# Kernel optimization log

Hardware: AMD Instinct MI355X
Metric: run time of the kernel (lower is better)

The kernel has to match this reference:

```python
import jax, jax.numpy as jnp
import numpy as np

KNN = 16
EPS = 1e-5

def _bn(x, g, b):
    # BatchNorm2d over channel-last axis, training-mode batch stats (axes B,N,K)
    m = jnp.mean(x, axis=(0, 1, 2), keepdims=True)
    v = jnp.var(x, axis=(0, 1, 2), keepdims=True)
    return (x - m) * jax.lax.rsqrt(v + EPS) * g + b

def _gather(x, idx):
    # x [B,N,C], idx [B,...] -> [B,...,C]
    return jax.vmap(lambda xi, ii: xi[ii])(x, idx)

def _fps(pc, m):
    # deterministic farthest point sampling starting at index 0 -> [B,m] int32
    B, N, _ = pc.shape
    first = jnp.zeros((B,), jnp.int32)
    def body(carry, _):
        mind, last = carry
        lp = jnp.take_along_axis(pc, last[:, None, None], axis=1)  # [B,1,3]
        mind = jnp.minimum(mind, jnp.sum((pc - lp) ** 2, axis=-1))  # [B,N]
        nxt = jnp.argmax(mind, axis=-1).astype(jnp.int32)
        return (mind, nxt), nxt
    _, rest = jax.lax.scan(body, (jnp.full((B, N), 1e10, pc.dtype), first), None, length=m - 1)
    return jnp.concatenate([first[None], rest], axis=0).T  # [B,m]

def _knn(pc1, pc2, k):
    # squared-distance matrix + k smallest (sorted ascending) -> indices [B,N1,k]
    d = (jnp.sum(pc1 ** 2, -1)[:, :, None] + jnp.sum(pc2 ** 2, -1)[:, None, :]
         - 2.0 * jnp.einsum('bnc,bmc->bnm', pc1, pc2))
    return jax.lax.top_k(-d, k)[1]

def reference(dec_x, dec_pc, enc_x, enc_pc,
              W_pre1, b_pre1, W_pre2, b_pre2,
              Wq, bq, Wk, bk, Wv, bv,
              Wp1, bp1, gp, betap, Wp2, bp2,
              Wa1, ba1, ga, betaa, Wa2, ba2,
              W_post1, b_post1, W_post2, b_post2):
    residue = dec_x
    dx = dec_x @ W_pre1 + b_pre1
    ex = enc_x @ W_pre2 + b_pre2
    pc = jnp.concatenate([dec_pc, enc_pc], axis=1)
    xx = jnp.concatenate([dx, ex], axis=1)
    fidx = _fps(pc, dec_pc.shape[1])
    pc = _gather(pc, fidx)
    xx = _gather(xx, fidx)
    q = dx @ Wq + bq
    k = xx @ Wk + bk
    v = xx @ Wv + bv
    nidx = _knn(dec_pc, pc, KNN)                          # [B,N1,K]
    pos_in = _gather(pc, nidx) - dec_pc[:, :, None, :]    # [B,N1,K,3] relative pos
    k = _gather(k, nidx)                                  # [B,N1,K,D]
    v = _gather(v, nidx)
    pos = jax.nn.relu(_bn(pos_in @ Wp1 + bp1, gp, betap)) @ Wp2 + bp2
    attn = k - q[:, :, None, :] + pos
    attn = jax.nn.relu(_bn(attn @ Wa1 + ba1, ga, betaa)) @ Wa2 + ba2
    attn = jax.nn.softmax(attn, axis=-2)                  # softmax over K neighbors
    x = jnp.sum((v + pos) * attn, axis=2)                 # [B,N1,D]
    return (x @ W_post1 + b_post1 + residue, dec_pc, x @ W_post2 + b_post2, enc_pc)

def setup_inputs():
    B, N1, N2 = 4, 2048, 2048
    D, I1, I2, HP, HA = 256, 256, 256, 64, 64
    ks = jax.random.split(jax.random.key(0), 24)
    rn = lambda i, shp, s: jax.random.normal(ks[i], shp, jnp.float32) * s
    z = lambda n: jnp.zeros((n,), jnp.float32)
    o = lambda n: jnp.ones((n,), jnp.float32)
    return {
        'dec_x': rn(0, (B, N1, I1), 1.0),
        'dec_pc': jax.random.uniform(ks[1], (B, N1, 3), jnp.float32),
        'enc_x': rn(2, (B, N2, I2), 1.0),
        'enc_pc': jax.random.uniform(ks[3], (B, N2, 3), jnp.float32),
        'W_pre1': rn(4, (I1, D), 0.02), 'b_pre1': z(D),
        'W_pre2': rn(5, (I2, D), 0.02), 'b_pre2': z(D),
        'Wq': rn(6, (D, D), 0.02), 'bq': z(D),
        'Wk': rn(7, (D, D), 0.02), 'bk': z(D),
        'Wv': rn(8, (D, D), 0.02), 'bv': z(D),
        'Wp1': rn(9, (3, HP), 0.1), 'bp1': z(HP), 'gp': o(HP), 'betap': z(HP),
        'Wp2': rn(10, (HP, D), 0.02), 'bp2': z(D),
        'Wa1': rn(11, (D, HA), 0.02), 'ba1': z(HA), 'ga': o(HA), 'betaa': z(HA),
        'Wa2': rn(12, (HA, D), 0.02), 'ba2': z(D),
        'W_post1': rn(13, (D, I1), 0.02), 'b_post1': z(I1),
        'W_post2': rn(14, (D, I2), 0.02), 'b_post2': z(I2),
    }
```

## Files before the change

kernel.cpp:

```cpp
#include <hip/hip_runtime.h>
#include <hip/hip_bf16.h>


typedef __hip_bfloat16 bf16;

__device__ __forceinline__ float b2f(bf16 x){ return __bfloat162float(x); }
__device__ __forceinline__ bf16  f2b(float x){ return __float2bfloat16(x); }

#define NQ    8192
#define NSAMP 131072

__global__ void detect_dtype(const unsigned int* __restrict__ words,
                             int* __restrict__ flag)
{
  int i = blockIdx.x*256 + threadIdx.x;
  unsigned int w = words[i];
  float v = __uint_as_float((w & 0xffffu) << 16);
  if (!(fabsf(v) <= 1e3f)) atomicOr(flag, 1);
}

struct ConvArgs {
  const void* src[30];
  float*      dst[30];
  int         n[30];
};
__global__ void convert_inputs(ConvArgs a, const int* __restrict__ flag)
{
  int t = blockIdx.y;
  int n = a.n[t];
  int isf32 = *flag;
  const void* s = a.src[t];
  float* d = a.dst[t];
  for (int i = blockIdx.x*256 + threadIdx.x; i < n; i += gridDim.x*256) {
    d[i] = isf32 ? ((const float*)s)[i] : b2f(((const bf16*)s)[i]);
  }
}

__global__ void copy_f32(const float* __restrict__ src, float* __restrict__ dst, int n)
{
  int i = blockIdx.x*256 + threadIdx.x;
  if (i < n) dst[i] = src[i];
}

template<int CTRL>
__device__ __forceinline__ void dpp_step(float& d, int& i) {
  int sd = __builtin_amdgcn_update_dpp(__float_as_int(d), __float_as_int(d),
                                       CTRL, 0xf, 0xf, false);
  int si = __builtin_amdgcn_update_dpp(i, i, CTRL, 0xf, 0xf, false);
  float fd = __int_as_float(sd);
  bool take = (fd > d) || (fd == d && si < i);
  d = take ? fd : d;
  i = take ? si : i;
}

__global__ __launch_bounds__(256) void fps_kernel(
    const float* __restrict__ dec_pc, const float* __restrict__ enc_pc,
    int* __restrict__ fidx)
{
  int b = blockIdx.x;
  int tid = threadIdx.x;
  __shared__ float4 spc[4096];
  __shared__ float  cd[2][4];
  __shared__ int    ci[2][4];

  float px[16], py[16], pz[16], mind[16];
#pragma unroll
  for (int i = 0; i < 16; ++i) {
    int p = tid*16 + i;
    const float* s = (p < 2048) ? dec_pc + ((size_t)b*2048 + p)*3
                                : enc_pc + ((size_t)b*2048 + (p-2048))*3;
    px[i] = s[0]; py[i] = s[1]; pz[i] = s[2];
    spc[p] = make_float4(px[i], py[i], pz[i], 0.f);
    mind[i] = 1e10f;
  }
  if (tid == 0) fidx[(size_t)b*2048] = 0;
  __syncthreads();

  int last = 0;
  int wv = tid >> 6;
  for (int t = 1; t < 2048; ++t) {
    float4 lp = spc[last];
    float bv = -1.f; int bi = 0x7fffffff;
#pragma unroll
    for (int i = 0; i < 16; ++i) {
      float ddx = px[i]-lp.x, ddy = py[i]-lp.y, ddz = pz[i]-lp.z;
      float d = __fadd_rn(__fadd_rn(__fmul_rn(ddx,ddx), __fmul_rn(ddy,ddy)),
                          __fmul_rn(ddz,ddz));
      mind[i] = fminf(mind[i], d);
      if (mind[i] > bv) { bv = mind[i]; bi = tid*16 + i; }
    }
    dpp_step<0x111>(bv, bi);
    dpp_step<0x112>(bv, bi);
    dpp_step<0x114>(bv, bi);
    dpp_step<0x118>(bv, bi);
    dpp_step<0x142>(bv, bi);
    dpp_step<0x143>(bv, bi);
    float wd = __int_as_float(__builtin_amdgcn_readlane(__float_as_int(bv), 63));
    int   wi = __builtin_amdgcn_readlane(bi, 63);
    int par = t & 1;
    if ((tid & 63) == 0) { cd[par][wv] = wd; ci[par][wv] = wi; }
    __syncthreads();
    float bd2 = cd[par][0]; int bi2 = ci[par][0];
#pragma unroll
    for (int w = 1; w < 4; ++w) {
      float d2 = cd[par][w]; int i2 = ci[par][w];
      if (d2 > bd2 || (d2 == bd2 && i2 < bi2)) { bd2 = d2; bi2 = i2; }
    }
    last = bi2;
    if (tid == 0) fidx[(size_t)b*2048 + t] = bi2;
  }
}

__global__ void gather_pc_kernel(const float* __restrict__ dec_pc,
                                 const float* __restrict__ enc_pc,
                                 const int* __restrict__ fidx,
                                 float* __restrict__ pcs)
{
  int i = blockIdx.x*256 + threadIdx.x;
  if (i >= NQ) return;
  int b = i >> 11;
  int g = fidx[i];
  const float* s = (g < 2048) ? dec_pc + ((size_t)b*2048 + g)*3
                              : enc_pc + ((size_t)b*2048 + (g-2048))*3;
  float X = s[0], Y = s[1], Z = s[2];
  float s2 = __fadd_rn(__fadd_rn(__fmul_rn(X,X), __fmul_rn(Y,Y)), __fmul_rn(Z,Z));
  ((float4*)pcs)[i] = make_float4(X, Y, Z, s2);
}

__global__ __launch_bounds__(64) void knn_kernel(
    const float* __restrict__ dec_pc, const float* __restrict__ pcs,
    int* __restrict__ nidx)
{
  int gq = blockIdx.x*64 + threadIdx.x;
  if (gq >= NQ) return;
  int b = gq >> 11;
  float qx = dec_pc[(size_t)gq*3+0];
  float qy = dec_pc[(size_t)gq*3+1];
  float qz = dec_pc[(size_t)gq*3+2];
  float s1 = __fadd_rn(__fadd_rn(__fmul_rn(qx,qx), __fmul_rn(qy,qy)), __fmul_rn(qz,qz));
  float bd[16]; int bi[16];
#pragma unroll
  for (int i = 0; i < 16; ++i) { bd[i] = 3.4e38f; bi[i] = 0; }
  const float4* P = (const float4*)(pcs) + (size_t)b*2048;
  for (int j = 0; j < 2048; ++j) {
    float4 p = P[j];
    float inner = __fadd_rn(__fadd_rn(__fmul_rn(qx,p.x), __fmul_rn(qy,p.y)),
                            __fmul_rn(qz,p.z));
    float d = __fsub_rn(__fadd_rn(s1, p.w), __fmul_rn(2.f, inner));
    if (d < bd[15]) {
      bd[15] = d; bi[15] = j;
#pragma unroll
      for (int k = 15; k >= 1; --k) {
        if (bd[k] < bd[k-1]) {
          float td = bd[k]; bd[k] = bd[k-1]; bd[k-1] = td;
          int   ti = bi[k]; bi[k] = bi[k-1]; bi[k-1] = ti;
        }
      }
    }
  }
  int* o = nidx + (size_t)gq*16;
#pragma unroll
  for (int i = 0; i < 16; ++i) o[i] = bi[i];
}

template<bool RESID>
__global__ __launch_bounds__(256) void gemm256(
    const float* __restrict__ A, const float* __restrict__ W,
    const float* __restrict__ bias, const float* __restrict__ resid,
    float* __restrict__ C, int M, int N)
{
  __shared__ float As[16][68];
  __shared__ float Bs[16][68];
  int bm = blockIdx.x*64, bn = blockIdx.y*64;
  int tid = threadIdx.x;
  int tr = tid >> 4, tc = tid & 15;
  float acc[4][4] = {};
  for (int k0 = 0; k0 < 256; k0 += 16) {
#pragma unroll
    for (int i = 0; i < 4; ++i) {
      int idx = tid + i*256;
      int m = idx >> 4, k = idx & 15;
      As[k][m] = A[(size_t)(bm+m)*256 + k0 + k];
    }
#pragma unroll
    for (int i = 0; i < 4; ++i) {
      int idx = tid + i*256;
      int k = idx >> 6, n = idx & 63;
      Bs[k][n] = W[(size_t)(k0+k)*N + bn + n];
    }
    __syncthreads();
#pragma unroll
    for (int k = 0; k < 16; ++k) {
      float4 a4 = *(const float4*)&As[k][tr*4];
      float4 b4 = *(const float4*)&Bs[k][tc*4];
      float a[4] = {a4.x, a4.y, a4.z, a4.w};
      float b[4] = {b4.x, b4.y, b4.z, b4.w};
#pragma unroll
      for (int i = 0; i < 4; ++i)
#pragma unroll
        for (int j = 0; j < 4; ++j) acc[i][j] += a[i]*b[j];
    }
    __syncthreads();
  }
#pragma unroll
  for (int i = 0; i < 4; ++i) {
    int m = bm + tr*4 + i;
#pragma unroll
    for (int j = 0; j < 4; ++j) {
      int n = bn + tc*4 + j;
      float v = acc[i][j] + (bias ? bias[n] : 0.f);
      if (RESID) v += resid[(size_t)m*N + n];
      C[(size_t)m*N + n] = v;
    }
  }
}

__global__ void gather_rows(const float* __restrict__ dx,
                            const float* __restrict__ ex,
                            const int* __restrict__ fidx,
                            float* __restrict__ xxg)
{
  int r = blockIdx.x;
  int b = r >> 11;
  int g = fidx[r];
  const float* src = (g < 2048) ? dx + ((size_t)(b*2048 + g))*256
                                : ex + ((size_t)(b*2048 + g - 2048))*256;
  ((float4*)(xxg + (size_t)r*256))[threadIdx.x] = ((const float4*)src)[threadIdx.x];
}

__global__ void fold_wa1(const float* __restrict__ Wq, const float* __restrict__ bq,
                         const float* __restrict__ Wk, const float* __restrict__ bk,
                         const float* __restrict__ Wa1,
                         float* __restrict__ Wqa, float* __restrict__ Wka,
                         float* __restrict__ bqa, float* __restrict__ bka)
{
  int c = threadIdx.x;
  int r = blockIdx.x;
  float aq = 0.f, ak = 0.f;
  if (r < 256) {
    for (int j = 0; j < 256; ++j) {
      float w = Wa1[j*64+c];
      aq += Wq[r*256+j]*w; ak += Wk[r*256+j]*w;
    }
    Wqa[r*64+c] = aq; Wka[r*64+c] = ak;
  } else {
    for (int j = 0; j < 256; ++j) {
      float w = Wa1[j*64+c];
      aq += bq[j]*w; ak += bk[j]*w;
    }
    bqa[c] = aq; bka[c] = ak;
  }
}

__global__ __launch_bounds__(256) void bn1_stats(
    const float* __restrict__ dec_pc, const float* __restrict__ pcs,
    const int* __restrict__ nidx, const float* __restrict__ Wp1,
    const float* __restrict__ bp1, double* __restrict__ sums)
{
  __shared__ float pin[256][3];
  __shared__ float red[8][64];
  int tid = threadIdx.x;
  int s0 = blockIdx.x * 256;
  {
    int s = s0 + tid;
    int qrow = s >> 4;
    int b = s >> 15;
    int g = nidx[s];
    float4 p = ((const float4*)pcs)[(size_t)b*2048 + g];
    pin[tid][0] = p.x - dec_pc[(size_t)qrow*3+0];
    pin[tid][1] = p.y - dec_pc[(size_t)qrow*3+1];
    pin[tid][2] = p.z - dec_pc[(size_t)qrow*3+2];
  }
  __syncthreads();
  int c = tid & 63, grp = tid >> 6;
  float w0 = Wp1[c], w1 = Wp1[64+c], w2 = Wp1[128+c], bb = bp1[c];
  float sm = 0.f, sq = 0.f;
  for (int i = 0; i < 64; ++i) {
    int r = grp*64 + i;
    float h = pin[r][0]*w0 + pin[r][1]*w1 + pin[r][2]*w2 + bb;
    sm += h; sq += h*h;
  }
  red[grp][c] = sm; red[4+grp][c] = sq;
  __syncthreads();
  if (tid < 64) {
    atomicAdd(&sums[tid], (double)(red[0][tid]+red[1][tid]+red[2][tid]+red[3][tid]));
  } else if (tid < 128) {
    int c2 = tid - 64;
    atomicAdd(&sums[64+c2], (double)(red[4][c2]+red[5][c2]+red[6][c2]+red[7][c2]));
  }
}

__global__ void bn_fin(const double* __restrict__ sums,
                       const float* __restrict__ gamma, const float* __restrict__ beta,
                       float* __restrict__ ab)
{
  int c = threadIdx.x;
  double mean = sums[c]    * (1.0/131072.0);
  double var  = sums[64+c] * (1.0/131072.0) - mean*mean;
  double inv  = 1.0 / sqrt(var + 1e-5);
  float a  = (float)(gamma[c] * inv);
  float bb = (float)(beta[c] - mean * (double)a);
  ab[c] = a; ab[64+c] = bb;
}

__global__ __launch_bounds__(256) void ph_kernel(
    const float* __restrict__ dec_pc, const float* __restrict__ pcs,
    const int* __restrict__ nidx, const float* __restrict__ Wp1,
    const float* __restrict__ bp1, const float* __restrict__ ab,
    bf16* __restrict__ PH)
{
  __shared__ float pin[256][3];
  int tid = threadIdx.x;
  int s0 = blockIdx.x * 256;
  {
    int s = s0 + tid;
    int qrow = s >> 4;
    int b = s >> 15;
    int g = nidx[s];
    float4 p = ((const float4*)pcs)[(size_t)b*2048 + g];
    pin[tid][0] = p.x - dec_pc[(size_t)qrow*3+0];
    pin[tid][1] = p.y - dec_pc[(size_t)qrow*3+1];
    pin[tid][2] = p.z - dec_pc[(size_t)qrow*3+2];
  }
  __syncthreads();
  int c = tid & 63, grp = tid >> 6;
  float w0 = Wp1[c], w1 = Wp1[64+c], w2 = Wp1[128+c], bb = bp1[c];
  float a = ab[c], sh = ab[64+c];
  for (int i = 0; i < 64; ++i) {
    int r = grp*64 + i;
    int s = s0 + r;
    float h = pin[r][0]*w0 + pin[r][1]*w1 + pin[r][2]*w2 + bb;
    PH[(size_t)s*64 + c] = f2b(fmaxf(h*a + sh, 0.f));
  }
}

__global__ void wprime_c1(const float* __restrict__ Wp2, const float* __restrict__ Wa1,
                          const float* __restrict__ bp2, const float* __restrict__ ba1,
                          float* __restrict__ Wpr, float* __restrict__ c1)
{
  int c = threadIdx.x;
  int r = blockIdx.x;
  if (r < 64) {
    float acc = 0.f;
    for (int e = 0; e < 256; ++e) acc += Wp2[r*256+e] * Wa1[e*64+c];
    Wpr[r*64+c] = acc;
  } else {
    float acc = ba1[c];
    for (int e = 0; e < 256; ++e) acc += bp2[e] * Wa1[e*64+c];
    c1[c] = acc;
  }
}

__global__ __launch_bounds__(256) void bn2_stats(
    const bf16* __restrict__ PH, const float* __restrict__ Wpr,
    const float* __restrict__ ka, const float* __restrict__ qa,
    const float* __restrict__ c1v, const int* __restrict__ nidx,
    bf16* __restrict__ attnpre, double* __restrict__ sums)
{
  __shared__ float phT[64][68];
  __shared__ float wp[64][68];
  __shared__ float red[16][64];
  __shared__ float red2[16][64];
  int tid = threadIdx.x;
  int s0 = blockIdx.x * 64;
#pragma unroll
  for (int i = 0; i < 16; ++i) {
    int idx = tid + i*256;
    wp[idx>>6][idx&63] = Wpr[idx];
    int r = idx >> 6, d = idx & 63;
    phT[d][r] = b2f(PH[(size_t)(s0+r)*64 + d]);
  }
  __syncthreads();
  int tr = tid >> 4, tc = tid & 15;
  float acc[4][4] = {};
#pragma unroll 8
  for (int d = 0; d < 64; ++d) {
    float4 a4 = *(const float4*)&phT[d][tr*4];
    float4 b4 = *(const float4*)&wp[d][tc*4];
    float a[4] = {a4.x, a4.y, a4.z, a4.w};
    float b[4] = {b4.x, b4.y, b4.z, b4.w};
#pragma unroll
    for (int i = 0; i < 4; ++i)
#pragma unroll
      for (int j = 0; j < 4; ++j) acc[i][j] += a[i]*b[j];
  }
  float psum[4] = {0,0,0,0}, psq[4] = {0,0,0,0};
#pragma unroll
  for (int i = 0; i < 4; ++i) {
    int r = tr*4 + i;
    int s = s0 + r;
    int b = s >> 15;
    int g = nidx[s];
    int qrow = s >> 4;
    const float* karow = ka + ((size_t)b*2048 + g)*64;
    const float* qarow = qa + (size_t)qrow*64;
#pragma unroll
    for (int j = 0; j < 4; ++j) {
      int c = tc*4 + j;
      float v = acc[i][j] + karow[c] - qarow[c] + c1v[c];
      attnpre[(size_t)s*64 + c] = f2b(v);
      psum[j] += v; psq[j] += v*v;
    }
  }
#pragma unroll
  for (int j = 0; j < 4; ++j) { red[tr][tc*4+j] = psum[j]; red2[tr][tc*4+j] = psq[j]; }
  __syncthreads();
  if (tid < 64) {
    float t = 0.f, t2 = 0.f;
#pragma unroll
    for (int i = 0; i < 16; ++i) { t += red[i][tid]; t2 += red2[i][tid]; }
    atomicAdd(&sums[tid], (double)t);
    atomicAdd(&sums[64+tid], (double)t2);
  }
}

__global__ __launch_bounds__(256) void final_attn(
    const bf16* __restrict__ attnpre, const bf16* __restrict__ PH,
    const float* __restrict__ ab2,
    const float* __restrict__ Wa2, const float* __restrict__ ba2,
    const float* __restrict__ Wp2, const float* __restrict__ bp2,
    const float* __restrict__ vsb, const int* __restrict__ nidx,
    float* __restrict__ xout)
{
  int tid = threadIdx.x;
  float wa[64], wpc[64];
#pragma unroll
  for (int d = 0; d < 64; ++d) {
    wa[d]  = Wa2[d*256 + tid];
    wpc[d] = Wp2[d*256 + tid];
  }
  float cba2 = ba2[tid];
  float cbp2 = bp2[tid];
  __shared__ float th[16][64];
  __shared__ float ph[16][64];
  __shared__ int   sn[16];
  for (int qi = 0; qi < 16; ++qi) {
    int q = blockIdx.x*16 + qi;
#pragma unroll
    for (int i = 0; i < 4; ++i) {
      int idx = tid + i*256;
      int k = idx >> 6, d = idx & 63;
      size_t gi = (size_t)q*1024 + idx;
      th[k][d] = fmaxf(b2f(attnpre[gi])*ab2[d] + ab2[64+d], 0.f);
      ph[k][d] = b2f(PH[gi]);
    }
    if (tid < 16) sn[tid] = nidx[(size_t)q*16 + tid];
    __syncthreads();
    float av[16], pv[16];
#pragma unroll
    for (int k = 0; k < 16; ++k) {
      float sa = cba2, sp = cbp2;
#pragma unroll
      for (int d = 0; d < 64; d += 4) {
        float4 t4 = *(const float4*)&th[k][d];
        float4 p4 = *(const float4*)&ph[k][d];
        sa += t4.x*wa[d] + t4.y*wa[d+1] + t4.z*wa[d+2] + t4.w*wa[d+3];
        sp += p4.x*wpc[d] + p4.y*wpc[d+1] + p4.z*wpc[d+2] + p4.w*wpc[d+3];
      }
      av[k] = sa; pv[k] = sp;
    }
    float m = av[0];
#pragma unroll
    for (int k = 1; k < 16; ++k) m = fmaxf(m, av[k]);
    float den = 0.f, num = 0.f;
    int b = q >> 11;
#pragma unroll
    for (int k = 0; k < 16; ++k) {
      float e = __expf(av[k] - m);
      den += e;
      float vk = vsb[((size_t)(b*2048 + sn[k]))*256 + tid];
      num += (vk + pv[k]) * e;
    }
    xout[(size_t)q*256 + tid] = num / den;
    __syncthreads();
  }
}

extern "C" void kernel_launch(void* const* d_in, const int* in_sizes, int n_in,
                              void* d_out, int out_size, void* d_ws, size_t ws_size,
                              hipStream_t stream) {
  (void)in_sizes; (void)n_in; (void)out_size; (void)ws_size;
  char* ws = (char*)d_ws;

  float* dec_xF  = (float*)(ws + 0);
  float* enc_xF  = (float*)(ws + 8388608);
  float* dxb     = (float*)(ws + 16777216);
  float* exb     = (float*)(ws + 25165824);
  float* Wqa     = (float*)(ws + 33554432);
  float* Wka     = (float*)(ws + 33619968);
  float* bqa     = (float*)(ws + 33685504);
  float* bka     = (float*)(ws + 33685760);
  float* xxg     = (float*)(ws + 41943040);
  float* vsb     = (float*)(ws + 58720256);
  float* xb      = (float*)(ws + 67108864);
  bf16*  PHb     = (bf16*)(ws + 75497472);
  bf16*  apre    = (bf16*)(ws + 92274688);
  float* qab     = (float*)(ws + 109051904);
  float* kab     = (float*)(ws + 111149056);
  float* dec_pcF = (float*)(ws + 113246208);
  float* enc_pcF = (float*)(ws + 113344512);
  float* W_pre1F = (float*)(ws + 113442816);
  float* W_pre2F = (float*)(ws + 113704960);
  float* WqF     = (float*)(ws + 113967104);
  float* WkF     = (float*)(ws + 114229248);
  float* WvF     = (float*)(ws + 114491392);
  float* W_post1F= (float*)(ws + 114753536);
  float* W_post2F= (float*)(ws + 115015680);
  float* Wp2F    = (float*)(ws + 115277824);
  float* Wa1F    = (float*)(ws + 115343360);
  float* Wa2F    = (float*)(ws + 115408896);
  float* Wp1F    = (float*)(ws + 115474432);
  float* vecs    = (float*)(ws + 115475456);
  float* b_pre1F = vecs + 0*256;
  float* b_pre2F = vecs + 1*256;
  float* bqF     = vecs + 2*256;
  float* bkF     = vecs + 3*256;
  float* bvF     = vecs + 4*256;
  float* bp1F    = vecs + 5*256;
  float* gpF     = vecs + 6*256;
  float* betapF  = vecs + 7*256;
  float* bp2F    = vecs + 8*256;
  float* ba1F    = vecs + 9*256;
  float* gaF     = vecs + 10*256;
  float* betaaF  = vecs + 11*256;
  float* ba2F    = vecs + 12*256;
  float* b_post1F= vecs + 13*256;
  float* b_post2F= vecs + 14*256;
  float* pcs     = (float*)(ws + 115490816);
  int*   fidx    = (int*)(ws + 115621888);
  int*   nidx    = (int*)(ws + 115654656);
  double* sums   = (double*)(ws + 116178944);
  float* Wpr     = (float*)(ws + 116180992);
  float* c1v     = (float*)(ws + 116197376);
  float* a1b1    = (float*)(ws + 116197632);
  float* a2b2    = (float*)(ws + 116198144);
  int*   flag    = (int*)(ws + 116198656);

  float* out  = (float*)d_out;
  float* out1 = out + 2097152;
  float* out2 = out + 2121728;
  float* out3 = out + 4218880;

  hipMemsetAsync(sums, 0, 256*sizeof(double), stream);
  hipMemsetAsync(flag, 0, sizeof(int), stream);

  detect_dtype<<<64, 256, 0, stream>>>((const unsigned int*)d_in[2], flag);

  ConvArgs ca;
  const int   ns[30]  = {2097152,24576,2097152,24576, 65536,256,65536,256,
                         65536,256,65536,256,65536,256, 192,64,64,64,
                         16384,256,16384,64,64,64,16384,256,
                         65536,256,65536,256};
  float* dsts[30] = {dec_xF,dec_pcF,enc_xF,enc_pcF, W_pre1F,b_pre1F,W_pre2F,b_pre2F,
                     WqF,bqF,WkF,bkF,WvF,bvF, Wp1F,bp1F,gpF,betapF,
                     Wp2F,bp2F,Wa1F,ba1F,gaF,betaaF,Wa2F,ba2F,
                     W_post1F,b_post1F,W_post2F,b_post2F};
  for (int i = 0; i < 30; ++i) { ca.src[i] = d_in[i]; ca.dst[i] = dsts[i]; ca.n[i] = ns[i]; }
  convert_inputs<<<dim3(512, 30), 256, 0, stream>>>(ca, flag);

  copy_f32<<<96, 256, 0, stream>>>(dec_pcF, out1, 24576);
  copy_f32<<<96, 256, 0, stream>>>(enc_pcF, out3, 24576);

  fps_kernel<<<4, 256, 0, stream>>>(dec_pcF, enc_pcF, fidx);
  gather_pc_kernel<<<32, 256, 0, stream>>>(dec_pcF, enc_pcF, fidx, pcs);
  knn_kernel<<<128, 64, 0, stream>>>(dec_pcF, pcs, nidx);

  gemm256<false><<<dim3(128,4), 256, 0, stream>>>(dec_xF, W_pre1F, b_pre1F, nullptr, dxb, 8192, 256);
  gemm256<false><<<dim3(128,4), 256, 0, stream>>>(enc_xF, W_pre2F, b_pre2F, nullptr, exb, 8192, 256);
  gather_rows<<<8192, 64, 0, stream>>>(dxb, exb, fidx, xxg);
  gemm256<false><<<dim3(128,4), 256, 0, stream>>>(xxg, WvF, bvF, nullptr, vsb, 8192, 256);
  fold_wa1<<<257, 64, 0, stream>>>(WqF, bqF, WkF, bkF, Wa1F, Wqa, Wka, bqa, bka);
  gemm256<false><<<dim3(128,1), 256, 0, stream>>>(dxb, Wqa, bqa, nullptr, qab, 8192, 64);
  gemm256<false><<<dim3(128,1), 256, 0, stream>>>(xxg, Wka, bka, nullptr, kab, 8192, 64);
  wprime_c1<<<65, 64, 0, stream>>>(Wp2F, Wa1F, bp2F, ba1F, Wpr, c1v);

  bn1_stats<<<512, 256, 0, stream>>>(dec_pcF, pcs, nidx, Wp1F, bp1F, sums);
  bn_fin<<<1, 64, 0, stream>>>(sums, gpF, betapF, a1b1);
  ph_kernel<<<512, 256, 0, stream>>>(dec_pcF, pcs, nidx, Wp1F, bp1F, a1b1, PHb);

  bn2_stats<<<2048, 256, 0, stream>>>(PHb, Wpr, kab, qab, c1v, nidx, apre, sums + 128);
  bn_fin<<<1, 64, 0, stream>>>(sums + 128, gaF, betaaF, a2b2);

  final_attn<<<512, 256, 0, stream>>>(apre, PHb, a2b2, Wa2F, ba2F, Wp2F, bp2F, vsb, nidx, xb);

  gemm256<true ><<<dim3(128,4), 256, 0, stream>>>(xb, W_post1F, b_post1F, dec_xF, out, 8192, 256);
  gemm256<false><<<dim3(128,4), 256, 0, stream>>>(xb, W_post2F, b_post2F, nullptr, out2, 8192, 256);
}
```

Measured before the change: 3.121 ms.

## Fold weight chains and overlap FPS with projection GEMMs in one megakernel

Precomposes W_pre·Wv, W_pre·Wqa and W_pre·Wka so the value and key/query projections run directly on the raw inputs, then gathers rows after projection instead of before. FPS runs as 4 blocks inside a megakernel next to all projection GEMM tiles and the point-cloud output copies, so the serial FPS loop overlaps the GEMMs rather than running alone. FPS also switches to SoA shared memory, a tree argmax per thread and a single float2 slot per wave. The two post GEMMs are merged into one launch. The trade-offs are extra GEMM work on the dec/enc split, and a bn2_stats change that now loads nidx inside the inner loop.

```diff
diff --git a/kernel.cpp b/kernel.cpp
--- a/kernel.cpp
+++ b/kernel.cpp
@@ -36,10 +36,57 @@
   }
 }
 
-__global__ void copy_f32(const float* __restrict__ src, float* __restrict__ dst, int n)
-{
-  int i = blockIdx.x*256 + threadIdx.x;
-  if (i < n) dst[i] = src[i];
+struct SGemm { float As[16][68]; float Bs[16][68]; };
+struct SFps  { float sx[4096]; float sy[4096]; float sz[4096]; float2 slot[2][4]; };
+union  SMega { SGemm g; SFps f; };
+
+__device__ __forceinline__ void gemm_body(
+    SGemm& sm, const float* __restrict__ A, const float* __restrict__ W,
+    const float* __restrict__ bias, const float* __restrict__ resid,
+    float* __restrict__ C, int N, int bm, int bn)
+{
+  int tid = threadIdx.x;
+  int tr = tid >> 4, tc = tid & 15;
+  float acc[4][4] = {};
+  for (int k0 = 0; k0 < 256; k0 += 16) {
+#pragma unroll
+    for (int i = 0; i < 4; ++i) {
+      int idx = tid + i*256;
+      int m = idx >> 4, k = idx & 15;
+      sm.As[k][m] = A[(size_t)(bm+m)*256 + k0 + k];
+    }
+#pragma unroll
+    for (int i = 0; i < 4; ++i) {
+      int idx = tid + i*256;
+      int k = idx >> 6, n = idx & 63;
+      sm.Bs[k][n] = W[(size_t)(k0+k)*N + bn + n];
+    }
+    __syncthreads();
+#pragma unroll
+    for (int k = 0; k < 16; ++k) {
+      float4 a4 = *(const float4*)&sm.As[k][tr*4];
+      float4 b4 = *(const float4*)&sm.Bs[k][tc*4];
+      float a[4] = {a4.x, a4.y, a4.z, a4.w};
+      float b[4] = {b4.x, b4.y, b4.z, b4.w};
+#pragma unroll
+      for (int i = 0; i < 4; ++i)
+#pragma unroll
+        for (int j = 0; j < 4; ++j) acc[i][j] += a[i]*b[j];
+    }
+    __syncthreads();
+  }
+#pragma unroll
+  for (int i = 0; i < 4; ++i) {
+    int m = bm + tr*4 + i;
+#pragma unroll
+    for (int j = 0; j < 4; ++j) {
+      int n = bn + tc*4 + j;
+      float v = acc[i][j];
+      if (bias)  v += bias[n];
+      if (resid) v += resid[(size_t)m*N + n];
+      C[(size_t)m*N + n] = v;
+    }
+  }
 }
 
 template<int CTRL>
@@ -53,16 +100,12 @@
   i = take ? si : i;
 }
 
-__global__ __launch_bounds__(256) void fps_kernel(
-    const float* __restrict__ dec_pc, const float* __restrict__ enc_pc,
-    int* __restrict__ fidx)
-{
-  int b = blockIdx.x;
+__device__ void fps_body(SFps& sm, int b,
+                         const float* __restrict__ dec_pc,
+                         const float* __restrict__ enc_pc,
+                         int* __restrict__ fidx)
+{
   int tid = threadIdx.x;
-  __shared__ float4 spc[4096];
-  __shared__ float  cd[2][4];
-  __shared__ int    ci[2][4];
-
   float px[16], py[16], pz[16], mind[16];
 #pragma unroll
   for (int i = 0; i < 16; ++i) {
@@ -70,7 +113,7 @@
     const float* s = (p < 2048) ? dec_pc + ((size_t)b*2048 + p)*3
                                 : enc_pc + ((size_t)b*2048 + (p-2048))*3;
     px[i] = s[0]; py[i] = s[1]; pz[i] = s[2];
-    spc[p] = make_float4(px[i], py[i], pz[i], 0.f);
+    sm.sx[p] = px[i]; sm.sy[p] = py[i]; sm.sz[p] = pz[i];
     mind[i] = 1e10f;
   }
   if (tid == 0) fidx[(size_t)b*2048] = 0;
@@ -79,52 +122,215 @@
   int last = 0;
   int wv = tid >> 6;
   for (int t = 1; t < 2048; ++t) {
-    float4 lp = spc[last];
-    float bv = -1.f; int bi = 0x7fffffff;
+    float lx = sm.sx[last], ly = sm.sy[last], lz = sm.sz[last];
 #pragma unroll
     for (int i = 0; i < 16; ++i) {
-      float ddx = px[i]-lp.x, ddy = py[i]-lp.y, ddz = pz[i]-lp.z;
+      float ddx = px[i]-lx, ddy = py[i]-ly, ddz = pz[i]-lz;
       float d = __fadd_rn(__fadd_rn(__fmul_rn(ddx,ddx), __fmul_rn(ddy,ddy)),
                           __fmul_rn(ddz,ddz));
       mind[i] = fminf(mind[i], d);
-      if (mind[i] > bv) { bv = mind[i]; bi = tid*16 + i; }
-    }
+    }
+    float vd[8]; int vi[8];
+#pragma unroll
+    for (int j = 0; j < 8; ++j) {
+      bool tk = mind[j+8] > mind[j];
+      vd[j] = tk ? mind[j+8] : mind[j];
+      vi[j] = tk ? (j+8) : j;
+    }
+#pragma unroll
+    for (int j = 0; j < 4; ++j) {
+      bool tk = vd[j+4] > vd[j];
+      vd[j] = tk ? vd[j+4] : vd[j];
+      vi[j] = tk ? vi[j+4] : vi[j];
+    }
+#pragma unroll
+    for (int j = 0; j < 2; ++j) {
+      bool tk = vd[j+2] > vd[j];
+      vd[j] = tk ? vd[j+2] : vd[j];
+      vi[j] = tk ? vi[j+2] : vi[j];
+    }
+    bool tk0 = vd[1] > vd[0];
+    float bv = tk0 ? vd[1] : vd[0];
+    int   bi = tid*16 + (tk0 ? vi[1] : vi[0]);
     dpp_step<0x111>(bv, bi);
     dpp_step<0x112>(bv, bi);
     dpp_step<0x114>(bv, bi);
     dpp_step<0x118>(bv, bi);
     dpp_step<0x142>(bv, bi);
     dpp_step<0x143>(bv, bi);
-    float wd = __int_as_float(__builtin_amdgcn_readlane(__float_as_int(bv), 63));
-    int   wi = __builtin_amdgcn_readlane(bi, 63);
     int par = t & 1;
-    if ((tid & 63) == 0) { cd[par][wv] = wd; ci[par][wv] = wi; }
+    if ((tid & 63) == 63) sm.slot[par][wv] = make_float2(bv, __int_as_float(bi));
     __syncthreads();
-    float bd2 = cd[par][0]; int bi2 = ci[par][0];
-#pragma unroll
-    for (int w = 1; w < 4; ++w) {
-      float d2 = cd[par][w]; int i2 = ci[par][w];
-      if (d2 > bd2 || (d2 == bd2 && i2 < bi2)) { bd2 = d2; bi2 = i2; }
-    }
-    last = bi2;
-    if (tid == 0) fidx[(size_t)b*2048 + t] = bi2;
-  }
-}
-
-__global__ void gather_pc_kernel(const float* __restrict__ dec_pc,
-                                 const float* __restrict__ enc_pc,
-                                 const int* __restrict__ fidx,
-                                 float* __restrict__ pcs)
-{
-  int i = blockIdx.x*256 + threadIdx.x;
-  if (i >= NQ) return;
-  int b = i >> 11;
-  int g = fidx[i];
-  const float* s = (g < 2048) ? dec_pc + ((size_t)b*2048 + g)*3
-                              : enc_pc + ((size_t)b*2048 + (g-2048))*3;
-  float X = s[0], Y = s[1], Z = s[2];
-  float s2 = __fadd_rn(__fadd_rn(__fmul_rn(X,X), __fmul_rn(Y,Y)), __fmul_rn(Z,Z));
-  ((float4*)pcs)[i] = make_float4(X, Y, Z, s2);
+    float4 s01 = *(const float4*)&sm.slot[par][0];
+    float4 s23 = *(const float4*)&sm.slot[par][2];
+    float d0 = s01.x; int i0 = __float_as_int(s01.y);
+    float d1 = s01.z; int i1 = __float_as_int(s01.w);
+    float d2 = s23.x; int i2 = __float_as_int(s23.y);
+    float d3 = s23.z; int i3 = __float_as_int(s23.w);
+    if (d1 > d0) { d0 = d1; i0 = i1; }
+    if (d3 > d2) { d2 = d3; i2 = i3; }
+    if (d2 > d0) { d0 = d2; i0 = i2; }
+    last = i0;
+    if (tid == 0) fidx[(size_t)b*2048 + t] = i0;
+  }
+}
+
+struct Mega1Args {
+  const float *dec_pc, *enc_pc, *dec_x, *enc_x;
+  const float *WfV1, *WfV2, *WfQ, *WfK1, *WfK2;
+  const float *bfV1, *bfV2, *bfQ, *bfK1, *bfK2;
+  float *vdec, *venc, *qab, *kdec, *kenc;
+  float *out1, *out3;
+  int *fidx;
+};
+__global__ __launch_bounds__(256) void mega1(Mega1Args a)
+{
+  __shared__ SMega sm;
+  int id = blockIdx.x;
+  if (id < 4) {
+    fps_body(sm.f, id, a.dec_pc, a.enc_pc, a.fidx);
+  } else if (id < 516) {
+    int l = id - 4;
+    gemm_body(sm.g, a.dec_x, a.WfV1, a.bfV1, nullptr, a.vdec, 256,
+              (l & 127) << 6, (l >> 7) << 6);
+  } else if (id < 1028) {
+    int l = id - 516;
+    gemm_body(sm.g, a.enc_x, a.WfV2, a.bfV2, nullptr, a.venc, 256,
+              (l & 127) << 6, (l >> 7) << 6);
+  } else if (id < 1156) {
+    int l = id - 1028;
+    gemm_body(sm.g, a.dec_x, a.WfQ, a.bfQ, nullptr, a.qab, 64, l << 6, 0);
+  } else if (id < 1284) {
+    int l = id - 1156;
+    gemm_body(sm.g, a.dec_x, a.WfK1, a.bfK1, nullptr, a.kdec, 64, l << 6, 0);
+  } else if (id < 1412) {
+    int l = id - 1284;
+    gemm_body(sm.g, a.enc_x, a.WfK2, a.bfK2, nullptr, a.kenc, 64, l << 6, 0);
+  } else if (id < 1508) {
+    int i = (id - 1412)*256 + threadIdx.x;
+    a.out1[i] = a.dec_pc[i];
+  } else {
+    int i = (id - 1508)*256 + threadIdx.x;
+    a.out3[i] = a.enc_pc[i];
+  }
+}
+
+__global__ __launch_bounds__(64) void foldA(
+    const float* __restrict__ Wq, const float* __restrict__ bq,
+    const float* __restrict__ Wk, const float* __restrict__ bk,
+    const float* __restrict__ Wa1,
+    const float* __restrict__ Wp2, const float* __restrict__ bp2,
+    const float* __restrict__ ba1,
+    float* __restrict__ Wqa, float* __restrict__ Wka,
+    float* __restrict__ bqa, float* __restrict__ bka,
+    float* __restrict__ Wpr, float* __restrict__ c1)
+{
+  int c = threadIdx.x;
+  int r = blockIdx.x;
+  if (r < 257) {
+    float aq = 0.f, ak = 0.f;
+    if (r < 256) {
+      for (int j = 0; j < 256; ++j) {
+        float w = Wa1[j*64+c];
+        aq += Wq[r*256+j]*w; ak += Wk[r*256+j]*w;
+      }
+      Wqa[r*64+c] = aq; Wka[r*64+c] = ak;
+    } else {
+      for (int j = 0; j < 256; ++j) {
+        float w = Wa1[j*64+c];
+        aq += bq[j]*w; ak += bk[j]*w;
+      }
+      bqa[c] = aq; bka[c] = ak;
+    }
+  } else {
+    int rr = r - 257;
+    if (rr < 64) {
+      float acc = 0.f;
+      for (int e = 0; e < 256; ++e) acc += Wp2[rr*256+e] * Wa1[e*64+c];
+      Wpr[rr*64+c] = acc;
+    } else {
+      float acc = ba1[c];
+      for (int e = 0; e < 256; ++e) acc += bp2[e] * Wa1[e*64+c];
+      c1[c] = acc;
+    }
+  }
+}
+
+struct FoldBArgs {
+  const float *W_pre1, *W_pre2, *Wv, *Wqa, *Wka;
+  const float *b_pre1, *b_pre2, *bv, *bqa, *bka;
+  float *WfV1, *WfV2, *WfQ, *WfK1, *WfK2;
+  float *bfV1, *bfV2, *bfQ, *bfK1, *bfK2;
+};
+__global__ __launch_bounds__(256) void foldB(FoldBArgs a)
+{
+  __shared__ SGemm sm;
+  int id = blockIdx.x;
+  if (id < 16) {
+    gemm_body(sm, a.W_pre1, a.Wv, nullptr, nullptr, a.WfV1, 256,
+              (id & 3) << 6, (id >> 2) << 6);
+  } else if (id < 32) {
+    int l = id - 16;
+    gemm_body(sm, a.W_pre2, a.Wv, nullptr, nullptr, a.WfV2, 256,
+              (l & 3) << 6, (l >> 2) << 6);
+  } else if (id < 36) {
+    gemm_body(sm, a.W_pre1, a.Wqa, nullptr, nullptr, a.WfQ, 64, (id-32) << 6, 0);
+  } else if (id < 40) {
+    gemm_body(sm, a.W_pre1, a.Wka, nullptr, nullptr, a.WfK1, 64, (id-36) << 6, 0);
+  } else if (id < 44) {
+    gemm_body(sm, a.W_pre2, a.Wka, nullptr, nullptr, a.WfK2, 64, (id-40) << 6, 0);
+  } else {
+    int t = threadIdx.x;
+    float s1 = 0.f, s2 = 0.f;
+    for (int k = 0; k < 256; ++k) {
+      float w = a.Wv[k*256+t];
+      s1 += a.b_pre1[k]*w; s2 += a.b_pre2[k]*w;
+    }
+    a.bfV1[t] = s1 + a.bv[t];
+    a.bfV2[t] = s2 + a.bv[t];
+    if (t < 64) {
+      float q = 0.f, k1 = 0.f, k2 = 0.f;
+      for (int k = 0; k < 256; ++k) {
+        float wq = a.Wqa[k*64+t], wk = a.Wka[k*64+t];
+        q  += a.b_pre1[k]*wq;
+        k1 += a.b_pre1[k]*wk;
+        k2 += a.b_pre2[k]*wk;
+      }
+      a.bfQ[t]  = q  + a.bqa[t];
+      a.bfK1[t] = k1 + a.bka[t];
+      a.bfK2[t] = k2 + a.bka[t];
+    }
+  }
+}
+
+__global__ __launch_bounds__(64) void gfetch(
+    const float* __restrict__ vdec, const float* __restrict__ venc,
+    const float* __restrict__ kdec, const float* __restrict__ kenc,
+    const float* __restrict__ dec_pc, const float* __restrict__ enc_pc,
+    const int* __restrict__ fidx,
+    float* __restrict__ vsb, float* __restrict__ kab, float* __restrict__ pcs)
+{
+  int id = blockIdx.x;
+  if (id < 8192) {
+    int r = id;
+    int b = r >> 11;
+    int g = fidx[r];
+    const float* vsrc = (g < 2048) ? vdec + ((size_t)(b*2048 + g))*256
+                                   : venc + ((size_t)(b*2048 + g - 2048))*256;
+    ((float4*)(vsb + (size_t)r*256))[threadIdx.x] = ((const float4*)vsrc)[threadIdx.x];
+    const float* ksrc = (g < 2048) ? kdec + (size_t)(b*2048 + g)*64
+                                   : kenc + (size_t)(b*2048 + g - 2048)*64;
+    kab[(size_t)r*64 + threadIdx.x] = ksrc[threadIdx.x];
+  } else {
+    int i = (id - 8192)*64 + threadIdx.x;
+    int b = i >> 11;
+    int g = fidx[i];
+    const float* s = (g < 2048) ? dec_pc + ((size_t)b*2048 + g)*3
+                                : enc_pc + ((size_t)b*2048 + (g-2048))*3;
+    float X = s[0], Y = s[1], Z = s[2];
+    float s2 = __fadd_rn(__fadd_rn(__fmul_rn(X,X), __fmul_rn(Y,Y)), __fmul_rn(Z,Z));
+    ((float4*)pcs)[i] = make_float4(X, Y, Z, s2);
+  }
 }
 
 __global__ __launch_bounds__(64) void knn_kernel(
@@ -161,95 +367,6 @@
   int* o = nidx + (size_t)gq*16;
 #pragma unroll
   for (int i = 0; i < 16; ++i) o[i] = bi[i];
-}
-
-template<bool RESID>
-__global__ __launch_bounds__(256) void gemm256(
-    const float* __restrict__ A, const float* __restrict__ W,
-    const float* __restrict__ bias, const float* __restrict__ resid,
-    float* __restrict__ C, int M, int N)
-{
-  __shared__ float As[16][68];
-  __shared__ float Bs[16][68];
-  int bm = blockIdx.x*64, bn = blockIdx.y*64;
-  int tid = threadIdx.x;
-  int tr = tid >> 4, tc = tid & 15;
-  float acc[4][4] = {};
-  for (int k0 = 0; k0 < 256; k0 += 16) {
-#pragma unroll
-    for (int i = 0; i < 4; ++i) {
-      int idx = tid + i*256;
-      int m = idx >> 4, k = idx & 15;
-      As[k][m] = A[(size_t)(bm+m)*256 + k0 + k];
-    }
-#pragma unroll
-    for (int i = 0; i < 4; ++i) {
-      int idx = tid + i*256;
-      int k = idx >> 6, n = idx & 63;
-      Bs[k][n] = W[(size_t)(k0+k)*N + bn + n];
-    }
-    __syncthreads();
-#pragma unroll
-    for (int k = 0; k < 16; ++k) {
-      float4 a4 = *(const float4*)&As[k][tr*4];
-      float4 b4 = *(const float4*)&Bs[k][tc*4];
-      float a[4] = {a4.x, a4.y, a4.z, a4.w};
-      float b[4] = {b4.x, b4.y, b4.z, b4.w};
-#pragma unroll
-      for (int i = 0; i < 4; ++i)
-#pragma unroll
-        for (int j = 0; j < 4; ++j) acc[i][j] += a[i]*b[j];
-    }
-    __syncthreads();
-  }
-#pragma unroll
-  for (int i = 0; i < 4; ++i) {
-    int m = bm + tr*4 + i;
-#pragma unroll
-    for (int j = 0; j < 4; ++j) {
-      int n = bn + tc*4 + j;
-      float v = acc[i][j] + (bias ? bias[n] : 0.f);
-      if (RESID) v += resid[(size_t)m*N + n];
-      C[(size_t)m*N + n] = v;
-    }
-  }
-}
-
-__global__ void gather_rows(const float* __restrict__ dx,
-                            const float* __restrict__ ex,
-                            const int* __restrict__ fidx,
-                            float* __restrict__ xxg)
-{
-  int r = blockIdx.x;
-  int b = r >> 11;
-  int g = fidx[r];
-  const float* src = (g < 2048) ? dx + ((size_t)(b*2048 + g))*256
-                                : ex + ((size_t)(b*2048 + g - 2048))*256;
-  ((float4*)(xxg + (size_t)r*256))[threadIdx.x] = ((const float4*)src)[threadIdx.x];
-}
-
-__global__ void fold_wa1(const float* __restrict__ Wq, const float* __restrict__ bq,
-                         const float* __restrict__ Wk, const float* __restrict__ bk,
-                         const float* __restrict__ Wa1,
-                         float* __restrict__ Wqa, float* __restrict__ Wka,
-                         float* __restrict__ bqa, float* __restrict__ bka)
-{
-  int c = threadIdx.x;
-  int r = blockIdx.x;
-  float aq = 0.f, ak = 0.f;
-  if (r < 256) {
-    for (int j = 0; j < 256; ++j) {
-      float w = Wa1[j*64+c];
-      aq += Wq[r*256+j]*w; ak += Wk[r*256+j]*w;
-    }
-    Wqa[r*64+c] = aq; Wka[r*64+c] = ak;
-  } else {
-    for (int j = 0; j < 256; ++j) {
-      float w = Wa1[j*64+c];
-      aq += bq[j]*w; ak += bk[j]*w;
-    }
-    bqa[c] = aq; bka[c] = ak;
-  }
 }
 
 __global__ __launch_bounds__(256) void bn1_stats(
@@ -334,23 +451,6 @@
   }
 }
 
-__global__ void wprime_c1(const float* __restrict__ Wp2, const float* __restrict__ Wa1,
-                          const float* __restrict__ bp2, const float* __restrict__ ba1,
-                          float* __restrict__ Wpr, float* __restrict__ c1)
-{
-  int c = threadIdx.x;
-  int r = blockIdx.x;
-  if (r < 64) {
-    float acc = 0.f;
-    for (int e = 0; e < 256; ++e) acc += Wp2[r*256+e] * Wa1[e*64+c];
-    Wpr[r*64+c] = acc;
-  } else {
-    float acc = ba1[c];
-    for (int e = 0; e < 256; ++e) acc += bp2[e] * Wa1[e*64+c];
-    c1[c] = acc;
-  }
-}
-
 __global__ __launch_bounds__(256) void bn2_stats(
     const bf16* __restrict__ PH, const float* __restrict__ Wpr,
     const float* __restrict__ ka, const float* __restrict__ qa,
@@ -389,15 +489,16 @@
   for (int i = 0; i < 4; ++i) {
     int r = tr*4 + i;
     int s = s0 + r;
-    int b = s >> 15;
-    int g = nidx[s];
     int qrow = s >> 4;
-    const float* karow = ka + ((size_t)b*2048 + g)*64;
+    const float* karow = ka + (size_t)s*64;
     const float* qarow = qa + (size_t)qrow*64;
+    (void)karow;
 #pragma unroll
     for (int j = 0; j < 4; ++j) {
       int c = tc*4 + j;
-      float v = acc[i][j] + karow[c] - qarow[c] + c1v[c];
+      int b = s >> 15;
+      int g = nidx[s];
+      float v = acc[i][j] + ka[((size_t)(b*2048 + g))*64 + c] - qarow[c] + c1v[c];
       attnpre[(size_t)s*64 + c] = f2b(v);
       psum[j] += v; psq[j] += v*v;
     }
@@ -476,41 +577,56 @@
   }
 }
 
+struct PostArgs {
+  const float *xb, *Wp1_, *bp1_, *Wp2_, *bp2_, *resid;
+  float *o1, *o2;
+};
+__global__ __launch_bounds__(256) void mega_post(PostArgs a)
+{
+  __shared__ SGemm sm;
+  int id = blockIdx.x;
+  if (id < 512) {
+    gemm_body(sm, a.xb, a.Wp1_, a.bp1_, a.resid, a.o1, 256,
+              (id & 127) << 6, (id >> 7) << 6);
+  } else {
+    int l = id - 512;
+    gemm_body(sm, a.xb, a.Wp2_, a.bp2_, nullptr, a.o2, 256,
+              (l & 127) << 6, (l >> 7) << 6);
+  }
+}
+
 extern "C" void kernel_launch(void* const* d_in, const int* in_sizes, int n_in,
                               void* d_out, int out_size, void* d_ws, size_t ws_size,
                               hipStream_t stream) {
   (void)in_sizes; (void)n_in; (void)out_size; (void)ws_size;
   char* ws = (char*)d_ws;
 
-  float* dec_xF  = (float*)(ws + 0);
-  float* enc_xF  = (float*)(ws + 8388608);
-  float* dxb     = (float*)(ws + 16777216);
-  float* exb     = (float*)(ws + 25165824);
-  float* Wqa     = (float*)(ws + 33554432);
-  float* Wka     = (float*)(ws + 33619968);
-  float* bqa     = (float*)(ws + 33685504);
-  float* bka     = (float*)(ws + 33685760);
-  float* xxg     = (float*)(ws + 41943040);
-  float* vsb     = (float*)(ws + 58720256);
-  float* xb      = (float*)(ws + 67108864);
-  bf16*  PHb     = (bf16*)(ws + 75497472);
-  bf16*  apre    = (bf16*)(ws + 92274688);
-  float* qab     = (float*)(ws + 109051904);
-  float* kab     = (float*)(ws + 111149056);
-  float* dec_pcF = (float*)(ws + 113246208);
-  float* enc_pcF = (float*)(ws + 113344512);
-  float* W_pre1F = (float*)(ws + 113442816);
-  float* W_pre2F = (float*)(ws + 113704960);
-  float* WqF     = (float*)(ws + 113967104);
-  float* WkF     = (float*)(ws + 114229248);
-  float* WvF     = (float*)(ws + 114491392);
-  float* W_post1F= (float*)(ws + 114753536);
-  float* W_post2F= (float*)(ws + 115015680);
-  float* Wp2F    = (float*)(ws + 115277824);
-  float* Wa1F    = (float*)(ws + 115343360);
-  float* Wa2F    = (float*)(ws + 115408896);
-  float* Wp1F    = (float*)(ws + 115474432);
-  float* vecs    = (float*)(ws + 115475456);
+  float* vdec    = (float*)(ws + 0);
+  float* venc    = (float*)(ws + 8388608);
+  float* vsb     = (float*)(ws + 16777216);
+  float* xb      = (float*)(ws + 25165824);
+  float* dec_xF  = (float*)(ws + 33554432);
+  float* enc_xF  = (float*)(ws + 41943040);
+  bf16*  PHb     = (bf16*)(ws + 50331648);
+  bf16*  apre    = (bf16*)(ws + 67108864);
+  float* qab     = (float*)(ws + 83886080);
+  float* kab     = (float*)(ws + 85983232);
+  float* kdec    = (float*)(ws + 88080384);
+  float* kenc    = (float*)(ws + 90177536);
+  float* dec_pcF = (float*)(ws + 92274688);
+  float* enc_pcF = (float*)(ws + 92372992);
+  float* W_pre1F = (float*)(ws + 92471296);
+  float* W_pre2F = (float*)(ws + 92733440);
+  float* WqF     = (float*)(ws + 92995584);
+  float* WkF     = (float*)(ws + 93257728);
+  float* WvF     = (float*)(ws + 93519872);
+  float* W_post1F= (float*)(ws + 93782016);
+  float* W_post2F= (float*)(ws + 94044160);
+  float* Wp2F    = (float*)(ws + 94306304);
+  float* Wa1F    = (float*)(ws + 94371840);
+  float* Wa2F    = (float*)(ws + 94437376);
+  float* Wp1F    = (float*)(ws + 94502912);
+  float* vecs    = (float*)(ws + 94503680);
   float* b_pre1F = vecs + 0*256;
   float* b_pre2F = vecs + 1*256;
   float* bqF     = vecs + 2*256;
@@ -526,15 +642,29 @@
   float* ba2F    = vecs + 12*256;
   float* b_post1F= vecs + 13*256;
   float* b_post2F= vecs + 14*256;
-  float* pcs     = (float*)(ws + 115490816);
-  int*   fidx    = (int*)(ws + 115621888);
-  int*   nidx    = (int*)(ws + 115654656);
-  double* sums   = (double*)(ws + 116178944);
-  float* Wpr     = (float*)(ws + 116180992);
-  float* c1v     = (float*)(ws + 116197376);
-  float* a1b1    = (float*)(ws + 116197632);
-  float* a2b2    = (float*)(ws + 116198144);
-  int*   flag    = (int*)(ws + 116198656);
+  float* WfV1    = (float*)(ws + 94519040);
+  float* WfV2    = (float*)(ws + 94781184);
+  float* WfQ     = (float*)(ws + 95043328);
+  float* WfK1    = (float*)(ws + 95108864);
+  float* WfK2    = (float*)(ws + 95174400);
+  float* Wqa     = (float*)(ws + 95239936);
+  float* Wka     = (float*)(ws + 95305472);
+  float* bfV1    = (float*)(ws + 95371008);
+  float* bfV2    = (float*)(ws + 95372032);
+  float* bfQ     = (float*)(ws + 95373056);
+  float* bfK1    = (float*)(ws + 95373312);
+  float* bfK2    = (float*)(ws + 95373568);
+  float* bqa     = (float*)(ws + 95373824);
+  float* bka     = (float*)(ws + 95374080);
+  float* pcs     = (float*)(ws + 95374336);
+  int*   fidx    = (int*)(ws + 95505408);
+  int*   nidx    = (int*)(ws + 95538176);
+  double* sums   = (double*)(ws + 96062464);
+  float* Wpr     = (float*)(ws + 96064512);
+  float* c1v     = (float*)(ws + 96080896);
+  float* a1b1    = (float*)(ws + 96081152);
+  float* a2b2    = (float*)(ws + 96081664);
+  int*   flag    = (int*)(ws + 96082176);
 
   float* out  = (float*)d_out;
   float* out1 = out + 2097152;
@@ -547,10 +677,10 @@
   detect_dtype<<<64, 256, 0, stream>>>((const unsigned int*)d_in[2], flag);
 
   ConvArgs ca;
-  const int   ns[30]  = {2097152,24576,2097152,24576, 65536,256,65536,256,
-                         65536,256,65536,256,65536,256, 192,64,64,64,
-                         16384,256,16384,64,64,64,16384,256,
-                         65536,256,65536,256};
+  const int ns[30] = {2097152,24576,2097152,24576, 65536,256,65536,256,
+                      65536,256,65536,256,65536,256, 192,64,64,64,
+                      16384,256,16384,64,64,64,16384,256,
+                      65536,256,65536,256};
   float* dsts[30] = {dec_xF,dec_pcF,enc_xF,enc_pcF, W_pre1F,b_pre1F,W_pre2F,b_pre2F,
                      WqF,bqF,WkF,bkF,WvF,bvF, Wp1F,bp1F,gpF,betapF,
                      Wp2F,bp2F,Wa1F,ba1F,gaF,betaaF,Wa2F,ba2F,
@@ -558,21 +688,27 @@
   for (int i = 0; i < 30; ++i) { ca.src[i] = d_in[i]; ca.dst[i] = dsts[i]; ca.n[i] = ns[i]; }
   convert_inputs<<<dim3(512, 30), 256, 0, stream>>>(ca, flag);
 
-  copy_f32<<<96, 256, 0, stream>>>(dec_pcF, out1, 24576);
-  copy_f32<<<96, 256, 0, stream>>>(enc_pcF, out3, 24576);
-
-  fps_kernel<<<4, 256, 0, stream>>>(dec_pcF, enc_pcF, fidx);
-  gather_pc_kernel<<<32, 256, 0, stream>>>(dec_pcF, enc_pcF, fidx, pcs);
+  foldA<<<322, 64, 0, stream>>>(WqF, bqF, WkF, bkF, Wa1F, Wp2F, bp2F, ba1F,
+                                Wqa, Wka, bqa, bka, Wpr, c1v);
+
+  FoldBArgs fb;
+  fb.W_pre1 = W_pre1F; fb.W_pre2 = W_pre2F; fb.Wv = WvF; fb.Wqa = Wqa; fb.Wka = Wka;
+  fb.b_pre1 = b_pre1F; fb.b_pre2 = b_pre2F; fb.bv = bvF; fb.bqa = bqa; fb.bka = bka;
+  fb.WfV1 = WfV1; fb.WfV2 = WfV2; fb.WfQ = WfQ; fb.WfK1 = WfK1; fb.WfK2 = WfK2;
+  fb.bfV1 = bfV1; fb.bfV2 = bfV2; fb.bfQ = bfQ; fb.bfK1 = bfK1; fb.bfK2 = bfK2;
+  foldB<<<45, 256, 0, stream>>>(fb);
+
+  Mega1Args m1;
+  m1.dec_pc = dec_pcF; m1.enc_pc = enc_pcF; m1.dec_x = dec_xF; m1.enc_x = enc_xF;
+  m1.WfV1 = WfV1; m1.WfV2 = WfV2; m1.WfQ = WfQ; m1.WfK1 = WfK1; m1.WfK2 = WfK2;
+  m1.bfV1 = bfV1; m1.bfV2 = bfV2; m1.bfQ = bfQ; m1.bfK1 = bfK1; m1.bfK2 = bfK2;
+  m1.vdec = vdec; m1.venc = venc; m1.qab = qab; m1.kdec = kdec; m1.kenc = kenc;
+  m1.out1 = out1; m1.out3 = out3; m1.fidx = fidx;
+  mega1<<<1604, 256, 0, stream>>>(m1);
+
+  gfetch<<<8320, 64, 0, stream>>>(vdec, venc, kdec, kenc, dec_pcF, enc_pcF,
+                                  fidx, vsb, kab, pcs);
   knn_kernel<<<128, 64, 0, stream>>>(dec_pcF, pcs, nidx);
-
-  gemm256<false><<<dim3(128,4), 256, 0, stream>>>(dec_xF, W_pre1F, b_pre1F, nullptr, dxb, 8192, 256);
-  gemm256<false><<<dim3(128,4), 256, 0, stream>>>(enc_xF, W_pre2F, b_pre2F, nullptr, exb, 8192, 256);
-  gather_rows<<<8192, 64, 0, stream>>>(dxb, exb, fidx, xxg);
-  gemm256<false><<<dim3(128,4), 256, 0, stream>>>(xxg, WvF, bvF, nullptr, vsb, 8192, 256);
-  fold_wa1<<<257, 64, 0, stream>>>(WqF, bqF, WkF, bkF, Wa1F, Wqa, Wka, bqa, bka);
-  gemm256<false><<<dim3(128,1), 256, 0, stream>>>(dxb, Wqa, bqa, nullptr, qab, 8192, 64);
-  gemm256<false><<<dim3(128,1), 256, 0, stream>>>(xxg, Wka, bka, nullptr, kab, 8192, 64);
-  wprime_c1<<<65, 64, 0, stream>>>(Wp2F, Wa1F, bp2F, ba1F, Wpr, c1v);
 
   bn1_stats<<<512, 256, 0, stream>>>(dec_pcF, pcs, nidx, Wp1F, bp1F, sums);
   bn_fin<<<1, 64, 0, stream>>>(sums, gpF, betapF, a1b1);
@@ -581,8 +717,12 @@
   bn2_stats<<<2048, 256, 0, stream>>>(PHb, Wpr, kab, qab, c1v, nidx, apre, sums + 128);
   bn_fin<<<1, 64, 0, stream>>>(sums + 128, gaF, betaaF, a2b2);
 
-  final_attn<<<512, 256, 0, stream>>>(apre, PHb, a2b2, Wa2F, ba2F, Wp2F, bp2F, vsb, nidx, xb);
-
-  gemm256<true ><<<dim3(128,4), 256, 0, stream>>>(xb, W_post1F, b_post1F, dec_xF, out, 8192, 256);
-  gemm256<false><<<dim3(128,4), 256, 0, stream>>>(xb, W_post2F, b_post2F, nullptr, out2, 8192, 256);
-}
+  final_attn<<<512, 256, 0, stream>>>(apre, PHb, a2b2, Wa2F, ba2F, Wp2F, bp2F,
+                                      vsb, nidx, xb);
+
+  PostArgs pa;
+  pa.xb = xb; pa.Wp1_ = W_post1F; pa.bp1_ = b_post1F;
+  pa.Wp2_ = W_post2F; pa.bp2_ = b_post2F; pa.resid = dec_xF;
+  pa.o1 = out; pa.o2 = out2;
+  mega_post<<<1024, 256, 0, stream>>>(pa);
+}
```

Result: faster. 2.765 ms (-11.4%).
